# Kernel tuning notes

Hardware: AMD Instinct MI355X
Metric: run time of the kernel (lower is better)

## Reference

```python
import jax, jax.numpy as jnp
import numpy as np

B, N1, N2, D, H = 16, 1024, 1024, 1024, 16
DH = D // H  # head dim = 64
NEG = jnp.float32(-1e30)  # mask fill value (avoids -inf NaNs, bf16-safe)


def setup_inputs() -> dict:
    key = jax.random.key(0)
    ks = jax.random.split(key, 8)
    s = 0.02
    q = jax.random.normal(ks[0], (B, N1, D), dtype=jnp.float32)
    x = jax.random.normal(ks[1], (B, N2, D), dtype=jnp.float32)
    Wq = jax.random.normal(ks[2], (D, D), dtype=jnp.float32) * s
    Wk = jax.random.normal(ks[3], (D, D), dtype=jnp.float32) * s
    Wv = jax.random.normal(ks[4], (D, D), dtype=jnp.float32) * s
    Wo = jax.random.normal(ks[5], (D, D), dtype=jnp.float32) * s
    bq = jnp.zeros((D,), jnp.float32)
    bk = jnp.zeros((D,), jnp.float32)
    bv = jnp.zeros((D,), jnp.float32)
    bo = jnp.zeros((D,), jnp.float32)
    adj_mat = jax.random.randint(ks[6], (N1, N2), 0, 2).astype(jnp.bool_)
    return {"q": q, "x": x, "Wq": Wq, "bq": bq, "Wk": Wk, "bk": bk,
            "Wv": Wv, "bv": bv, "Wo": Wo, "bo": bo, "adj_mat": adj_mat}


def reference(q, x, Wq, bq, Wk, bk, Wv, bv, Wo, bo, adj_mat):
    b = q.shape[0]
    # QKV projections (torch Linear: y = x @ W.T + b), split into heads
    qh = (q @ Wq.T + bq).reshape(b, N1, H, DH).transpose(0, 2, 1, 3)  # [B,H,N1,DH]
    kh = (x @ Wk.T + bk).reshape(b, N2, H, DH).transpose(0, 2, 1, 3)  # [B,H,N2,DH]
    vh = (x @ Wv.T + bv).reshape(b, N2, H, DH).transpose(0, 2, 1, 3)  # [B,H,N2,DH]
    # masked SDPA with fixed adjacency mask (broadcast over batch & heads)
    scale = jnp.asarray(DH, qh.dtype) ** -0.5
    scores = jnp.einsum("bhqd,bhkd->bhqk", qh, kh) * scale           # [B,H,N1,N2]
    scores = jnp.where(adj_mat, scores, NEG)
    attn = jax.nn.softmax(scores, axis=-1)
    o = jnp.einsum("bhqk,bhkd->bhqd", attn, vh)                      # [B,H,N1,DH]
    o = o.transpose(0, 2, 1, 3).reshape(b, N1, D)
    return o @ Wo.T + bo
```

## Files before the change

### kernel.cpp

```cpp
#include <hip/hip_runtime.h>


typedef float f32x4 __attribute__((ext_vector_type(4)));
typedef float f32x16 __attribute__((ext_vector_type(16)));
typedef __bf16 bf16x8 __attribute__((ext_vector_type(8)));

#define QSCALE 0.18033688f

__device__ __forceinline__ unsigned short f2bf(float f) {
    unsigned u = __builtin_bit_cast(unsigned, f);
    unsigned r = u + 0x7fffu + ((u >> 16) & 1u);
    return (unsigned short)(r >> 16);
}
__device__ __forceinline__ unsigned pk2(float a, float b) {
    return (unsigned)f2bf(a) | ((unsigned)f2bf(b) << 16);
}

__global__ __launch_bounds__(256) void cvt_bf16(const float* __restrict__ s0,
                                                unsigned short* __restrict__ d0,
                                                const float* __restrict__ s1,
                                                unsigned short* __restrict__ d1) {
    const float* src = blockIdx.y ? s1 : s0;
    unsigned short* dst = blockIdx.y ? d1 : d0;
    const int idx = blockIdx.x * 256 + threadIdx.x;
    float4 a = ((const float4*)src)[idx * 2];
    float4 b = ((const float4*)src)[idx * 2 + 1];
    uint4 u;
    u.x = pk2(a.x, a.y); u.y = pk2(a.z, a.w);
    u.z = pk2(b.x, b.y); u.w = pk2(b.z, b.w);
    ((uint4*)dst)[idx] = u;
}

__global__ __launch_bounds__(256) void cvt_w4(const float* __restrict__ W0,
                                              const float* __restrict__ W1,
                                              const float* __restrict__ W2,
                                              const float* __restrict__ W3,
                                              unsigned short* __restrict__ o0,
                                              unsigned short* __restrict__ o1,
                                              unsigned short* __restrict__ o2,
                                              unsigned short* __restrict__ o3) {
    const float* s = (blockIdx.y == 0) ? W0 : (blockIdx.y == 1) ? W1
                   : (blockIdx.y == 2) ? W2 : W3;
    unsigned short* d = (blockIdx.y == 0) ? o0 : (blockIdx.y == 1) ? o1
                      : (blockIdx.y == 2) ? o2 : o3;
    const int idx = blockIdx.x * 256 + threadIdx.x;
    float4 a = ((const float4*)s)[idx * 2];
    float4 b = ((const float4*)s)[idx * 2 + 1];
    uint4 u;
    u.x = pk2(a.x, a.y); u.y = pk2(a.z, a.w);
    u.z = pk2(b.x, b.y); u.w = pk2(b.z, b.w);
    ((uint4*)d)[idx] = u;
}

template <int OUTM_CONST>
__device__ __forceinline__ void gemm_body(const unsigned short* __restrict__ A,
                                          const unsigned short* __restrict__ W,
                                          const float* __restrict__ bias,
                                          void* __restrict__ Cp,
                                          float scale, int b2, int outm_rt) {
    constexpr int N = 1024, K = 1024;
    __shared__ unsigned short As[2][128 * 64];
    __shared__ unsigned short Bs[2][128 * 64];

    const int t    = threadIdx.x;
    const int wave = t >> 6;
    const int lane = t & 63;
    const int xcd  = b2 & 7;
    const int jj   = b2 >> 3;
    const int n0   = (jj & 7) * 128;
    const int m0   = (xcd * 16 + (jj >> 3)) * 128;
    const int wr   = (wave >> 1) * 64;
    const int wc   = (wave & 1) * 64;
    const int lm   = lane & 15;
    const int quad = lane >> 4;

    int aoff[4], boff[4];
#pragma unroll
    for (int i = 0; i < 4; i++) {
        const int slot = wave * 256 + i * 64 + lane;
        const int r = slot >> 3;
        const int csrc = (slot & 7) ^ (r & 7);
        aoff[i] = (m0 + r) * K + csrc * 8;
        boff[i] = (n0 + r) * K + csrc * 8;
    }

    auto STAGE = [&](int cb, int k0) {
#pragma unroll
        for (int i = 0; i < 4; i++) {
            __builtin_amdgcn_global_load_lds(
                (const __attribute__((address_space(1))) unsigned int*)(A + aoff[i] + k0),
                (__attribute__((address_space(3))) unsigned int*)((char*)&As[cb][0] + wave * 4096 + i * 1024),
                16, 0, 0);
            __builtin_amdgcn_global_load_lds(
                (const __attribute__((address_space(1))) unsigned int*)(W + boff[i] + k0),
                (__attribute__((address_space(3))) unsigned int*)((char*)&Bs[cb][0] + wave * 4096 + i * 1024),
                16, 0, 0);
        }
    };

    f32x4 acc[4][4] = {};

    STAGE(0, 0);
    __syncthreads();

    int cur = 0;
    for (int k0 = 0; k0 < K; k0 += 64) {
        if (k0 + 64 < K) STAGE(cur ^ 1, k0 + 64);

        bf16x8 af[2][4], bfr[2][4];
#pragma unroll
        for (int ks = 0; ks < 2; ks++)
#pragma unroll
            for (int i = 0; i < 4; i++) {
                const int pos = ((ks * 4 + quad) ^ (lm & 7)) * 16;
                af[ks][i]  = *(const bf16x8*)((const char*)&As[cur][0] + (wr + i * 16 + lm) * 128 + pos);
                bfr[ks][i] = *(const bf16x8*)((const char*)&Bs[cur][0] + (wc + i * 16 + lm) * 128 + pos);
            }
        __builtin_amdgcn_s_setprio(1);
#pragma unroll
        for (int ks = 0; ks < 2; ks++)
#pragma unroll
            for (int i = 0; i < 4; i++)
#pragma unroll
                for (int j = 0; j < 4; j++)
                    acc[i][j] = __builtin_amdgcn_mfma_f32_16x16x32_bf16(af[ks][i], bfr[ks][j],
                                                                        acc[i][j], 0, 0, 0);
        __builtin_amdgcn_s_setprio(0);
        __syncthreads();
        cur ^= 1;
    }

    const int outm = (OUTM_CONST >= 0) ? OUTM_CONST : outm_rt;

#pragma unroll
    for (int i = 0; i < 4; i++) {
        const int row = m0 + wr + i * 16 + quad * 4;
#pragma unroll
        for (int j = 0; j < 4; j++) {
            const int col = n0 + wc + j * 16 + lm;
            const float bb = bias[col];
            if (outm == 2) {
                const int bi = row >> 10, n2 = row & 1023;
                const int hh = col >> 6, dh = col & 63;
                uint2 pkd;
                pkd.x = pk2((acc[i][j][0] + bb) * scale, (acc[i][j][1] + bb) * scale);
                pkd.y = pk2((acc[i][j][2] + bb) * scale, (acc[i][j][3] + bb) * scale);
                *(uint2*)&((unsigned short*)Cp)[((size_t)((bi * 16 + hh) * 64 + dh) << 10) + n2] = pkd;
            } else if (outm == 0) {
#pragma unroll
                for (int rr = 0; rr < 4; rr++)
                    ((unsigned short*)Cp)[(size_t)(row + rr) * N + col] =
                        f2bf((acc[i][j][rr] + bb) * scale);
            } else {
#pragma unroll
                for (int rr = 0; rr < 4; rr++)
                    ((float*)Cp)[(size_t)(row + rr) * N + col] = (acc[i][j][rr] + bb) * scale;
            }
        }
    }
}

__global__ __launch_bounds__(256, 2) void gemm_qkv(const unsigned short* __restrict__ qb,
                                                   const unsigned short* __restrict__ xb,
                                                   const unsigned short* __restrict__ Wqb,
                                                   const unsigned short* __restrict__ Wkb,
                                                   const unsigned short* __restrict__ Wvb,
                                                   const float* __restrict__ bq,
                                                   const float* __restrict__ bk,
                                                   const float* __restrict__ bv,
                                                   unsigned short* __restrict__ Qo,
                                                   unsigned short* __restrict__ Ko,
                                                   unsigned short* __restrict__ Vo) {
    const int bid = blockIdx.x;
    const int z   = bid >> 10;
    const int b2  = bid & 1023;
    const unsigned short* A = (z == 0) ? qb : xb;
    const unsigned short* W = (z == 0) ? Wqb : (z == 1) ? Wkb : Wvb;
    const float* bias       = (z == 0) ? bq : (z == 1) ? bk : bv;
    void* Cp                = (z == 0) ? (void*)Qo : (z == 1) ? (void*)Ko : (void*)Vo;
    const float scale       = (z == 0) ? QSCALE : 1.0f;
    gemm_body<-1>(A, W, bias, Cp, scale, b2, (z == 2) ? 2 : 0);
}

template <int OUTM>
__global__ __launch_bounds__(256, 2) void gemm2(const unsigned short* __restrict__ A,
                                                const unsigned short* __restrict__ W,
                                                const float* __restrict__ bias,
                                                void* __restrict__ Cp,
                                                float scale) {
    gemm_body<OUTM>(A, W, bias, Cp, scale, blockIdx.x, OUTM);
}

template <bool A_BF16, int OUTM>
__global__ __launch_bounds__(256) void gemm_bt(const void* __restrict__ Ap,
                                               const float* __restrict__ Wp,
                                               const float* __restrict__ bias,
                                               void* __restrict__ Cp,
                                               float scale) {
    constexpr int N = 1024, K = 1024;
    __shared__ unsigned short As[128 * 40];
    __shared__ unsigned short Bs[128 * 40];

    const int t    = threadIdx.x;
    const int n0   = blockIdx.x * 128;
    const int m0   = blockIdx.y * 128;
    const int wave = t >> 6;
    const int lane = t & 63;
    const int wr   = (wave >> 1) * 64;
    const int wc   = (wave & 1) * 64;
    const int lm   = lane & 15;
    const int quad = lane >> 4;
    const int kfr  = quad * 8;
    const int srow  = t >> 1;
    const int shalf = (t & 1) * 16;

    f32x4 acc[4][4] = {};

    for (int k0 = 0; k0 < K; k0 += 32) {
        {
            unsigned short* dst = &As[srow * 40 + shalf];
            if constexpr (A_BF16) {
                const unsigned short* pa =
                    (const unsigned short*)Ap + (size_t)(m0 + srow) * K + k0 + shalf;
                *(uint4*)dst       = *(const uint4*)pa;
                *(uint4*)(dst + 8) = *(const uint4*)(pa + 8);
            } else {
                const float* pa = (const float*)Ap + (size_t)(m0 + srow) * K + k0 + shalf;
                float4 f0 = *(const float4*)(pa + 0);
                float4 f1 = *(const float4*)(pa + 4);
                float4 f2 = *(const float4*)(pa + 8);
                float4 f3 = *(const float4*)(pa + 12);
                uint4 u0, u1;
                u0.x = pk2(f0.x, f0.y); u0.y = pk2(f0.z, f0.w);
                u0.z = pk2(f1.x, f1.y); u0.w = pk2(f1.z, f1.w);
                u1.x = pk2(f2.x, f2.y); u1.y = pk2(f2.z, f2.w);
                u1.z = pk2(f3.x, f3.y); u1.w = pk2(f3.z, f3.w);
                *(uint4*)dst       = u0;
                *(uint4*)(dst + 8) = u1;
            }
        }
        {
            const float* pb = Wp + (size_t)(n0 + srow) * K + k0 + shalf;
            float4 f0 = *(const float4*)(pb + 0);
            float4 f1 = *(const float4*)(pb + 4);
            float4 f2 = *(const float4*)(pb + 8);
            float4 f3 = *(const float4*)(pb + 12);
            uint4 u0, u1;
            u0.x = pk2(f0.x, f0.y); u0.y = pk2(f0.z, f0.w);
            u0.z = pk2(f1.x, f1.y); u0.w = pk2(f1.z, f1.w);
            u1.x = pk2(f2.x, f2.y); u1.y = pk2(f2.z, f2.w);
            u1.z = pk2(f3.x, f3.y); u1.w = pk2(f3.z, f3.w);
            unsigned short* dst = &Bs[srow * 40 + shalf];
            *(uint4*)dst       = u0;
            *(uint4*)(dst + 8) = u1;
        }
        __syncthreads();

        bf16x8 af[4], bfr[4];
#pragma unroll
        for (int i = 0; i < 4; i++)
            af[i] = *reinterpret_cast<const bf16x8*>(&As[(wr + i * 16 + lm) * 40 + kfr]);
#pragma unroll
        for (int j = 0; j < 4; j++)
            bfr[j] = *reinterpret_cast<const bf16x8*>(&Bs[(wc + j * 16 + lm) * 40 + kfr]);
#pragma unroll
        for (int i = 0; i < 4; i++)
#pragma unroll
            for (int j = 0; j < 4; j++)
                acc[i][j] = __builtin_amdgcn_mfma_f32_16x16x32_bf16(af[i], bfr[j],
                                                                    acc[i][j], 0, 0, 0);
        __syncthreads();
    }

#pragma unroll
    for (int i = 0; i < 4; i++) {
        const int row = m0 + wr + i * 16 + quad * 4;
#pragma unroll
        for (int j = 0; j < 4; j++) {
            const int col = n0 + wc + j * 16 + lm;
            const float bb = bias[col];
#pragma unroll
            for (int rr = 0; rr < 4; rr++) {
                const float v = (acc[i][j][rr] + bb) * scale;
                const int m = row + rr;
                if constexpr (OUTM == 0) {
                    ((unsigned short*)Cp)[(size_t)m * N + col] = f2bf(v);
                } else if constexpr (OUTM == 1) {
                    ((float*)Cp)[(size_t)m * N + col] = v;
                } else {
                    const int bi = m >> 10, n2 = m & 1023;
                    const int hh = col >> 6, dh = col & 63;
                    ((unsigned short*)Cp)[((size_t)((bi * 16 + hh) * 64 + dh) << 10) + n2] =
                        f2bf(v);
                }
            }
        }
    }
}

__global__ __launch_bounds__(256) void pack_adj(const int* __restrict__ adj,
                                                unsigned* __restrict__ adjm) {
    const int idx = blockIdx.x * 256 + threadIdx.x;
    const int* src = adj + (size_t)idx * 32;
    unsigned w = 0;
#pragma unroll
    for (int i = 0; i < 32; i++) w |= (src[i] != 0 ? 1u : 0u) << i;
    adjm[idx] = w;
}

__global__ __launch_bounds__(256, 3) void attn_kernel(const unsigned short* __restrict__ Q,
                                                      const unsigned short* __restrict__ K,
                                                      const unsigned short* __restrict__ Vt,
                                                      const unsigned* __restrict__ adjm,
                                                      unsigned short* __restrict__ O) {
    __shared__ unsigned short Kbuf[2][4096];
    __shared__ unsigned short Vbuf[2][4096];

    const int t    = threadIdx.x;
    const int wave = t >> 6;
    const int lane = t & 63;
    const int l32  = lane & 31;
    const int hi   = lane >> 5;

    const int bid   = blockIdx.x;
    const int xcd   = bid & 7;
    const int jj    = bid >> 3;
    const int group = xcd * 32 + (jj >> 3);
    const int q0    = (jj & 7) * 128;
    const int h     = group & 15;
    const int b     = group >> 4;

    const int qrow = q0 + wave * 32 + l32;

    int    ldofs[2];
    size_t kofs[2], vofs[2];
#pragma unroll
    for (int i = 0; i < 2; i++) {
        const int slot = i * 256 + t;
        const int r    = slot >> 3;
        const int cs   = (slot & 7) ^ (r & 7);
        ldofs[i] = slot * 16;
        kofs[i]  = (size_t)(b * 1024 + r) * 1024 + h * 64 + cs * 8;
        vofs[i]  = ((size_t)((b * 16 + h) * 64 + r) << 10) + cs * 8;
    }

    bf16x8 aq[4];
    {
        const unsigned short* qp =
            Q + ((size_t)(b * 1024 + qrow) * 1024 + h * 64 + hi * 8);
#pragma unroll
        for (int s = 0; s < 4; s++)
            aq[s] = __builtin_bit_cast(bf16x8, *(const uint4*)(qp + s * 16));
    }

    bf16x8 bones;
    {
        uint4 u; u.x = 0x3F803F80u; u.y = u.x; u.z = u.x; u.w = u.x;
        bones = __builtin_bit_cast(bf16x8, u);
    }

    f32x16 of0 = {}, of1 = {}, ol = {};

    auto STAGE = [&](int bi, int c) {
        const size_t j0 = (size_t)c * 64;
#pragma unroll
        for (int i = 0; i < 2; i++) {
            __builtin_amdgcn_global_load_lds(
                (const __attribute__((address_space(1))) unsigned int*)(K + kofs[i] + j0 * 1024),
                (__attribute__((address_space(3))) unsigned int*)((char*)&Kbuf[bi][0] + ldofs[i]),
                16, 0, 0);
            __builtin_amdgcn_global_load_lds(
                (const __attribute__((address_space(1))) unsigned int*)(Vt + vofs[i] + j0),
                (__attribute__((address_space(3))) unsigned int*)((char*)&Vbuf[bi][0] + ldofs[i]),
                16, 0, 0);
        }
    };

    STAGE(0, 0);
    __syncthreads();

    int bi = 0;
    for (int c = 0; c < 16; ++c) {
        const uint2 mw = *(const uint2*)&adjm[(size_t)qrow * 32 + c * 2];

        if (c < 15) STAGE(bi ^ 1, c + 1);

        f32x16 sf[2] = {{}, {}};
        __builtin_amdgcn_s_setprio(1);
#pragma unroll
        for (int f = 0; f < 2; f++)
#pragma unroll
            for (int s = 0; s < 4; s++) {
                const int pos = ((2 * s + hi) ^ (l32 & 7)) * 16;
                const bf16x8 kf =
                    *(const bf16x8*)((const char*)&Kbuf[bi][0] + (f * 32 + l32) * 128 + pos);
                sf[f] = __builtin_amdgcn_mfma_f32_32x32x16_bf16(kf, aq[s], sf[f], 0, 0, 0);
            }
        __builtin_amdgcn_s_setprio(0);

        unsigned d[2][4][2];
#pragma unroll
        for (int f = 0; f < 2; f++) {
            const unsigned wh = ((f == 0) ? mw.x : mw.y) >> (hi * 4);
            float p[16];
#pragma unroll
            for (int r = 0; r < 16; r++) {
                const unsigned bit = (wh >> ((r & 3) + 8 * (r >> 2))) & 1u;
                p[r] = __builtin_amdgcn_exp2f(bit ? sf[f][r] : -1e30f);
            }
#pragma unroll
            for (int a = 0; a < 4; a++)
#pragma unroll
                for (int bb = 0; bb < 2; bb++) {
                    unsigned dd;
                    asm("v_cvt_pk_bf16_f32 %0, %1, %2"
                        : "=v"(dd) : "v"(p[4 * a + 2 * bb]), "v"(p[4 * a + 2 * bb + 1]));
                    d[f][a][bb] = dd;
                }
        }

        bf16x8 tA[4];
#pragma unroll
        for (int s = 0; s < 4; s++) {
            const int f = s >> 1, sg = s & 1;
            unsigned A0 = d[f][2 * sg][0], B0 = d[f][2 * sg + 1][0];
            unsigned A1 = d[f][2 * sg][1], B1 = d[f][2 * sg + 1][1];
            asm("v_permlane32_swap_b32 %0, %1" : "+v"(A0), "+v"(B0));
            asm("v_permlane32_swap_b32 %0, %1" : "+v"(A1), "+v"(B1));
            uint4 td; td.x = A0; td.y = A1; td.z = B0; td.w = B1;
            tA[s] = __builtin_bit_cast(bf16x8, td);
        }

        __builtin_amdgcn_s_setprio(1);
#pragma unroll
        for (int s = 0; s < 4; s++) {
            const int pos = ((2 * s + hi) ^ (l32 & 7)) * 16;
            const bf16x8 v0 = *(const bf16x8*)((const char*)&Vbuf[bi][0] + l32 * 128 + pos);
            const bf16x8 v1 = *(const bf16x8*)((const char*)&Vbuf[bi][0] + (32 + l32) * 128 + pos);
            of0 = __builtin_amdgcn_mfma_f32_32x32x16_bf16(tA[s], v0, of0, 0, 0, 0);
            of1 = __builtin_amdgcn_mfma_f32_32x32x16_bf16(tA[s], v1, of1, 0, 0, 0);
            ol  = __builtin_amdgcn_mfma_f32_32x32x16_bf16(tA[s], bones, ol, 0, 0, 0);
        }
        __builtin_amdgcn_s_setprio(0);

        __syncthreads();
        bi ^= 1;
    }

#pragma unroll
    for (int r = 0; r < 16; r++) {
        const float iv = 1.0f / ol[r];
        const size_t row = (size_t)(b * 1024 + q0 + wave * 32 +
                                    (r & 3) + 8 * (r >> 2) + 4 * hi);
        unsigned short* op = O + row * 1024 + h * 64 + l32;
        op[0]  = f2bf(of0[r] * iv);
        op[32] = f2bf(of1[r] * iv);
    }
}

extern "C" void kernel_launch(void* const* d_in, const int* in_sizes, int n_in,
                              void* d_out, int out_size, void* d_ws, size_t ws_size,
                              hipStream_t stream) {
    const float* q  = (const float*)d_in[0];
    const float* x  = (const float*)d_in[1];
    const float* Wq = (const float*)d_in[2];
    const float* bq = (const float*)d_in[3];
    const float* Wk = (const float*)d_in[4];
    const float* bk = (const float*)d_in[5];
    const float* Wv = (const float*)d_in[6];
    const float* bv = (const float*)d_in[7];
    const float* Wo = (const float*)d_in[8];
    const float* bo = (const float*)d_in[9];
    const int* adj  = (const int*)d_in[10];
    float* out = (float*)d_out;

    const size_t MB = 1024 * 1024;
    char* w = (char*)d_ws;

    dim3 tb(256);
    const size_t FULL_WS = 168 * MB + 128 * 1024;

    if (ws_size >= FULL_WS) {
        unsigned short* qb  = (unsigned short*)(w);
        unsigned short* xb  = (unsigned short*)(w + 32 * MB);
        unsigned short* Wqb = (unsigned short*)(w + 64 * MB);
        unsigned short* Wkb = (unsigned short*)(w + 66 * MB);
        unsigned short* Wvb = (unsigned short*)(w + 68 * MB);
        unsigned short* Wob = (unsigned short*)(w + 70 * MB);
        unsigned short* Qb  = (unsigned short*)(w + 72 * MB);
        unsigned short* Kb  = (unsigned short*)(w + 104 * MB);
        unsigned short* Vtb = (unsigned short*)(w + 136 * MB);
        unsigned* adjm      = (unsigned*)(w + 168 * MB);
        unsigned short* Ob  = qb;

        hipLaunchKernelGGL(cvt_bf16, dim3(8192, 2), tb, 0, stream, q, qb, x, xb);
        hipLaunchKernelGGL(cvt_w4, dim3(512, 4), tb, 0, stream, Wq, Wk, Wv, Wo,
                           Wqb, Wkb, Wvb, Wob);
        hipLaunchKernelGGL(pack_adj, dim3(128), tb, 0, stream, adj, adjm);

        hipLaunchKernelGGL(gemm_qkv, dim3(3072), tb, 0, stream,
                           qb, xb, Wqb, Wkb, Wvb, bq, bk, bv, Qb, Kb, Vtb);
        hipLaunchKernelGGL(attn_kernel, dim3(2048), tb, 0, stream, Qb, Kb, Vtb, adjm, Ob);
        hipLaunchKernelGGL((gemm2<1>), dim3(1024), tb, 0, stream, Ob, Wob, bo, (void*)out, 1.0f);
    } else {
        unsigned short* Qb  = (unsigned short*)(w);
        unsigned short* Kb  = (unsigned short*)(w + 32 * MB);
        unsigned short* Vtb = (unsigned short*)(w + 64 * MB);
        unsigned short* Ob  = (unsigned short*)(w + 96 * MB);
        unsigned* adjm      = (unsigned*)(w + 128 * MB);

        hipLaunchKernelGGL(pack_adj, dim3(128), tb, 0, stream, adj, adjm);
        hipLaunchKernelGGL((gemm_bt<false, 0>), dim3(8, 128), tb, 0, stream,
                           (const void*)q, Wq, bq, (void*)Qb, QSCALE);
        hipLaunchKernelGGL((gemm_bt<false, 0>), dim3(8, 128), tb, 0, stream,
                           (const void*)x, Wk, bk, (void*)Kb, 1.0f);
        hipLaunchKernelGGL((gemm_bt<false, 2>), dim3(8, 128), tb, 0, stream,
                           (const void*)x, Wv, bv, (void*)Vtb, 1.0f);
        hipLaunchKernelGGL(attn_kernel, dim3(2048), tb, 0, stream, Qb, Kb, Vtb, adjm, Ob);
        hipLaunchKernelGGL((gemm_bt<true, 1>), dim3(8, 128), tb, 0, stream,
                           (const void*)Ob, Wo, bo, (void*)out, 1.0f);
    }
}
```

Before: 449.7 us.

## Fuse fp32-to-bf16 activation conversion into QKV GEMM and merge prep kernels

The separate pass that converts q and x to bf16 is removed. The QKV GEMM now loads fp32 activation tiles into registers, converts them, and writes swizzled bf16 into LDS after the MFMA loop. The weight conversion and adjacency packing are merged into one prep kernel to cut launches. This drops a 64MB read plus 64MB write round trip, but the GEMM now reads fp32 A tiles twice over (once per N-tile column, so 8x) and relies on register staging instead of async LDS loads for A.

```diff
diff --git a/kernel.cpp b/kernel.cpp
--- a/kernel.cpp
+++ b/kernel.cpp
@@ -16,48 +16,43 @@
     return (unsigned)f2bf(a) | ((unsigned)f2bf(b) << 16);
 }
 
-__global__ __launch_bounds__(256) void cvt_bf16(const float* __restrict__ s0,
-                                                unsigned short* __restrict__ d0,
-                                                const float* __restrict__ s1,
-                                                unsigned short* __restrict__ d1) {
-    const float* src = blockIdx.y ? s1 : s0;
-    unsigned short* dst = blockIdx.y ? d1 : d0;
-    const int idx = blockIdx.x * 256 + threadIdx.x;
-    float4 a = ((const float4*)src)[idx * 2];
-    float4 b = ((const float4*)src)[idx * 2 + 1];
-    uint4 u;
-    u.x = pk2(a.x, a.y); u.y = pk2(a.z, a.w);
-    u.z = pk2(b.x, b.y); u.w = pk2(b.z, b.w);
-    ((uint4*)dst)[idx] = u;
-}
-
-__global__ __launch_bounds__(256) void cvt_w4(const float* __restrict__ W0,
-                                              const float* __restrict__ W1,
-                                              const float* __restrict__ W2,
-                                              const float* __restrict__ W3,
-                                              unsigned short* __restrict__ o0,
-                                              unsigned short* __restrict__ o1,
-                                              unsigned short* __restrict__ o2,
-                                              unsigned short* __restrict__ o3) {
-    const float* s = (blockIdx.y == 0) ? W0 : (blockIdx.y == 1) ? W1
-                   : (blockIdx.y == 2) ? W2 : W3;
-    unsigned short* d = (blockIdx.y == 0) ? o0 : (blockIdx.y == 1) ? o1
-                      : (blockIdx.y == 2) ? o2 : o3;
-    const int idx = blockIdx.x * 256 + threadIdx.x;
-    float4 a = ((const float4*)s)[idx * 2];
-    float4 b = ((const float4*)s)[idx * 2 + 1];
-    uint4 u;
-    u.x = pk2(a.x, a.y); u.y = pk2(a.z, a.w);
-    u.z = pk2(b.x, b.y); u.w = pk2(b.z, b.w);
-    ((uint4*)d)[idx] = u;
-}
-
-template <int OUTM_CONST>
-__device__ __forceinline__ void gemm_body(const unsigned short* __restrict__ A,
-                                          const unsigned short* __restrict__ W,
-                                          const float* __restrict__ bias,
-                                          void* __restrict__ Cp,
-                                          float scale, int b2, int outm_rt) {
+__global__ __launch_bounds__(256) void prep(const float* __restrict__ W0,
+                                            const float* __restrict__ W1,
+                                            const float* __restrict__ W2,
+                                            const float* __restrict__ W3,
+                                            unsigned short* __restrict__ o0,
+                                            unsigned short* __restrict__ o1,
+                                            unsigned short* __restrict__ o2,
+                                            unsigned short* __restrict__ o3,
+                                            const int* __restrict__ adj,
+                                            unsigned* __restrict__ adjm) {
+    const int bid = blockIdx.x;
+    if (bid < 2048) {
+        const int wsel = bid >> 9;
+        const float* s = (wsel == 0) ? W0 : (wsel == 1) ? W1 : (wsel == 2) ? W2 : W3;
+        unsigned short* d = (wsel == 0) ? o0 : (wsel == 1) ? o1 : (wsel == 2) ? o2 : o3;
+        const int idx = (bid & 511) * 256 + threadIdx.x;
+        float4 a = ((const float4*)s)[idx * 2];
+        float4 b = ((const float4*)s)[idx * 2 + 1];
+        uint4 u;
+        u.x = pk2(a.x, a.y); u.y = pk2(a.z, a.w);
+        u.z = pk2(b.x, b.y); u.w = pk2(b.z, b.w);
+        ((uint4*)d)[idx] = u;
+    } else {
+        const int idx = (bid - 2048) * 256 + threadIdx.x;
+        const int* src = adj + (size_t)idx * 32;
+        unsigned w = 0;
+#pragma unroll
+        for (int i = 0; i < 32; i++) w |= (src[i] != 0 ? 1u : 0u) << i;
+        adjm[idx] = w;
+    }
+}
+
+__device__ __forceinline__ void gemm_f32a_body(const float* __restrict__ A,
+                                               const unsigned short* __restrict__ W,
+                                               const float* __restrict__ bias,
+                                               void* __restrict__ Cp,
+                                               float scale, int b2, int outm) {
     constexpr int N = 1024, K = 1024;
     __shared__ unsigned short As[2][128 * 64];
     __shared__ unsigned short Bs[2][128 * 64];
@@ -74,38 +69,61 @@
     const int lm   = lane & 15;
     const int quad = lane >> 4;
 
-    int aoff[4], boff[4];
+    const int srow = t >> 1;
+    const int colh = (t & 1) * 32;
+    const float* abase = A + (size_t)(m0 + srow) * K + colh;
+
+    int boff[4];
 #pragma unroll
     for (int i = 0; i < 4; i++) {
         const int slot = wave * 256 + i * 64 + lane;
         const int r = slot >> 3;
         const int csrc = (slot & 7) ^ (r & 7);
-        aoff[i] = (m0 + r) * K + csrc * 8;
         boff[i] = (n0 + r) * K + csrc * 8;
     }
 
-    auto STAGE = [&](int cb, int k0) {
-#pragma unroll
-        for (int i = 0; i < 4; i++) {
-            __builtin_amdgcn_global_load_lds(
-                (const __attribute__((address_space(1))) unsigned int*)(A + aoff[i] + k0),
-                (__attribute__((address_space(3))) unsigned int*)((char*)&As[cb][0] + wave * 4096 + i * 1024),
-                16, 0, 0);
+    float4 fa[8];
+    auto LOADA = [&](int k0) {
+#pragma unroll
+        for (int i = 0; i < 8; i++)
+            fa[i] = *(const float4*)(abase + k0 + i * 4);
+    };
+    auto WRITEA = [&](int cb) {
+        unsigned short* dst = &As[cb][srow * 64];
+#pragma unroll
+        for (int cc = 0; cc < 4; cc++) {
+            uint4 u;
+            u.x = pk2(fa[cc * 2].x, fa[cc * 2].y);
+            u.y = pk2(fa[cc * 2].z, fa[cc * 2].w);
+            u.z = pk2(fa[cc * 2 + 1].x, fa[cc * 2 + 1].y);
+            u.w = pk2(fa[cc * 2 + 1].z, fa[cc * 2 + 1].w);
+            const int c = (colh >> 3) + cc;
+            *(uint4*)(dst + ((c ^ (srow & 7)) * 8)) = u;
+        }
+    };
+    auto STAGEW = [&](int cb, int k0) {
+#pragma unroll
+        for (int i = 0; i < 4; i++)
             __builtin_amdgcn_global_load_lds(
                 (const __attribute__((address_space(1))) unsigned int*)(W + boff[i] + k0),
                 (__attribute__((address_space(3))) unsigned int*)((char*)&Bs[cb][0] + wave * 4096 + i * 1024),
                 16, 0, 0);
-        }
     };
 
     f32x4 acc[4][4] = {};
 
-    STAGE(0, 0);
+    LOADA(0);
+    STAGEW(0, 0);
+    WRITEA(0);
     __syncthreads();
 
     int cur = 0;
     for (int k0 = 0; k0 < K; k0 += 64) {
-        if (k0 + 64 < K) STAGE(cur ^ 1, k0 + 64);
+        const bool more = (k0 + 64 < K);
+        if (more) {
+            LOADA(k0 + 64);
+            STAGEW(cur ^ 1, k0 + 64);
+        }
 
         bf16x8 af[2][4], bfr[2][4];
 #pragma unroll
@@ -126,11 +144,11 @@
                     acc[i][j] = __builtin_amdgcn_mfma_f32_16x16x32_bf16(af[ks][i], bfr[ks][j],
                                                                         acc[i][j], 0, 0, 0);
         __builtin_amdgcn_s_setprio(0);
+
+        if (more) WRITEA(cur ^ 1);
         __syncthreads();
         cur ^= 1;
     }
-
-    const int outm = (OUTM_CONST >= 0) ? OUTM_CONST : outm_rt;
 
 #pragma unroll
     for (int i = 0; i < 4; i++) {
@@ -146,22 +164,18 @@
                 pkd.x = pk2((acc[i][j][0] + bb) * scale, (acc[i][j][1] + bb) * scale);
                 pkd.y = pk2((acc[i][j][2] + bb) * scale, (acc[i][j][3] + bb) * scale);
                 *(uint2*)&((unsigned short*)Cp)[((size_t)((bi * 16 + hh) * 64 + dh) << 10) + n2] = pkd;
-            } else if (outm == 0) {
+            } else {
 #pragma unroll
                 for (int rr = 0; rr < 4; rr++)
                     ((unsigned short*)Cp)[(size_t)(row + rr) * N + col] =
                         f2bf((acc[i][j][rr] + bb) * scale);
-            } else {
-#pragma unroll
-                for (int rr = 0; rr < 4; rr++)
-                    ((float*)Cp)[(size_t)(row + rr) * N + col] = (acc[i][j][rr] + bb) * scale;
             }
         }
     }
 }
 
-__global__ __launch_bounds__(256, 2) void gemm_qkv(const unsigned short* __restrict__ qb,
-                                                   const unsigned short* __restrict__ xb,
+__global__ __launch_bounds__(256, 2) void gemm_qkv(const float* __restrict__ q,
+                                                   const float* __restrict__ x,
                                                    const unsigned short* __restrict__ Wqb,
                                                    const unsigned short* __restrict__ Wkb,
                                                    const unsigned short* __restrict__ Wvb,
@@ -174,21 +188,104 @@
     const int bid = blockIdx.x;
     const int z   = bid >> 10;
     const int b2  = bid & 1023;
-    const unsigned short* A = (z == 0) ? qb : xb;
+    const float* A          = (z == 0) ? q : x;
     const unsigned short* W = (z == 0) ? Wqb : (z == 1) ? Wkb : Wvb;
     const float* bias       = (z == 0) ? bq : (z == 1) ? bk : bv;
     void* Cp                = (z == 0) ? (void*)Qo : (z == 1) ? (void*)Ko : (void*)Vo;
     const float scale       = (z == 0) ? QSCALE : 1.0f;
-    gemm_body<-1>(A, W, bias, Cp, scale, b2, (z == 2) ? 2 : 0);
-}
-
-template <int OUTM>
-__global__ __launch_bounds__(256, 2) void gemm2(const unsigned short* __restrict__ A,
-                                                const unsigned short* __restrict__ W,
-                                                const float* __restrict__ bias,
-                                                void* __restrict__ Cp,
-                                                float scale) {
-    gemm_body<OUTM>(A, W, bias, Cp, scale, blockIdx.x, OUTM);
+    gemm_f32a_body(A, W, bias, Cp, scale, b2, (z == 2) ? 2 : 0);
+}
+
+__global__ __launch_bounds__(256, 2) void gemm_o(const unsigned short* __restrict__ A,
+                                                 const unsigned short* __restrict__ W,
+                                                 const float* __restrict__ bias,
+                                                 float* __restrict__ Cp,
+                                                 float scale) {
+    constexpr int N = 1024, K = 1024;
+    __shared__ unsigned short As[2][128 * 64];
+    __shared__ unsigned short Bs[2][128 * 64];
+
+    const int t    = threadIdx.x;
+    const int wave = t >> 6;
+    const int lane = t & 63;
+    const int b2   = blockIdx.x;
+    const int xcd  = b2 & 7;
+    const int jj   = b2 >> 3;
+    const int n0   = (jj & 7) * 128;
+    const int m0   = (xcd * 16 + (jj >> 3)) * 128;
+    const int wr   = (wave >> 1) * 64;
+    const int wc   = (wave & 1) * 64;
+    const int lm   = lane & 15;
+    const int quad = lane >> 4;
+
+    int aoff[4], boff[4];
+#pragma unroll
+    for (int i = 0; i < 4; i++) {
+        const int slot = wave * 256 + i * 64 + lane;
+        const int r = slot >> 3;
+        const int csrc = (slot & 7) ^ (r & 7);
+        aoff[i] = (m0 + r) * K + csrc * 8;
+        boff[i] = (n0 + r) * K + csrc * 8;
+    }
+
+    auto STAGE = [&](int cb, int k0) {
+#pragma unroll
+        for (int i = 0; i < 4; i++) {
+            __builtin_amdgcn_global_load_lds(
+                (const __attribute__((address_space(1))) unsigned int*)(A + aoff[i] + k0),
+                (__attribute__((address_space(3))) unsigned int*)((char*)&As[cb][0] + wave * 4096 + i * 1024),
+                16, 0, 0);
+            __builtin_amdgcn_global_load_lds(
+                (const __attribute__((address_space(1))) unsigned int*)(W + boff[i] + k0),
+                (__attribute__((address_space(3))) unsigned int*)((char*)&Bs[cb][0] + wave * 4096 + i * 1024),
+                16, 0, 0);
+        }
+    };
+
+    f32x4 acc[4][4] = {};
+
+    STAGE(0, 0);
+    __syncthreads();
+
+    int cur = 0;
+    for (int k0 = 0; k0 < K; k0 += 64) {
+        if (k0 + 64 < K) STAGE(cur ^ 1, k0 + 64);
+
+        bf16x8 af[2][4], bfr[2][4];
+#pragma unroll
+        for (int ks = 0; ks < 2; ks++)
+#pragma unroll
+            for (int i = 0; i < 4; i++) {
+                const int pos = ((ks * 4 + quad) ^ (lm & 7)) * 16;
+                af[ks][i]  = *(const bf16x8*)((const char*)&As[cur][0] + (wr + i * 16 + lm) * 128 + pos);
+                bfr[ks][i] = *(const bf16x8*)((const char*)&Bs[cur][0] + (wc + i * 16 + lm) * 128 + pos);
+            }
+        __builtin_amdgcn_s_setprio(1);
+#pragma unroll
+        for (int ks = 0; ks < 2; ks++)
+#pragma unroll
+            for (int i = 0; i < 4; i++)
+#pragma unroll
+                for (int j = 0; j < 4; j++)
+                    acc[i][j] = __builtin_amdgcn_mfma_f32_16x16x32_bf16(af[ks][i], bfr[ks][j],
+                                                                        acc[i][j], 0, 0, 0);
+        __builtin_amdgcn_s_setprio(0);
+        __syncthreads();
+        cur ^= 1;
+    }
+
+#pragma unroll
+    for (int i = 0; i < 4; i++) {
+        const int row = m0 + wr + i * 16 + quad * 4;
+#pragma unroll
+        for (int j = 0; j < 4; j++) {
+            const int col = n0 + wc + j * 16 + lm;
+            const float bb = bias[col];
+#pragma unroll
+            for (int rr = 0; rr < 4; rr++)
+                Cp[(size_t)(row + rr) * N + col] = (acc[i][j][rr] + bb) * scale;
+        }
+    }
 }
 
 template <bool A_BF16, int OUTM>
@@ -481,8 +578,7 @@
     const size_t FULL_WS = 168 * MB + 128 * 1024;
 
     if (ws_size >= FULL_WS) {
-        unsigned short* qb  = (unsigned short*)(w);
-        unsigned short* xb  = (unsigned short*)(w + 32 * MB);
+        unsigned short* Ob  = (unsigned short*)(w);
         unsigned short* Wqb = (unsigned short*)(w + 64 * MB);
         unsigned short* Wkb = (unsigned short*)(w + 66 * MB);
         unsigned short* Wvb = (unsigned short*)(w + 68 * MB);
@@ -491,17 +587,13 @@
         unsigned short* Kb  = (unsigned short*)(w + 104 * MB);
         unsigned short* Vtb = (unsigned short*)(w + 136 * MB);
         unsigned* adjm      = (unsigned*)(w + 168 * MB);
-        unsigned short* Ob  = qb;
-
-        hipLaunchKernelGGL(cvt_bf16, dim3(8192, 2), tb, 0, stream, q, qb, x, xb);
-        hipLaunchKernelGGL(cvt_w4, dim3(512, 4), tb, 0, stream, Wq, Wk, Wv, Wo,
-                           Wqb, Wkb, Wvb, Wob);
-        hipLaunchKernelGGL(pack_adj, dim3(128), tb, 0, stream, adj, adjm);
-
+
+        hipLaunchKernelGGL(prep, dim3(2176), tb, 0, stream,
+                           Wq, Wk, Wv, Wo, Wqb, Wkb, Wvb, Wob, adj, adjm);
         hipLaunchKernelGGL(gemm_qkv, dim3(3072), tb, 0, stream,
-                           qb, xb, Wqb, Wkb, Wvb, bq, bk, bv, Qb, Kb, Vtb);
+                           q, x, Wqb, Wkb, Wvb, bq, bk, bv, Qb, Kb, Vtb);
         hipLaunchKernelGGL(attn_kernel, dim3(2048), tb, 0, stream, Qb, Kb, Vtb, adjm, Ob);
-        hipLaunchKernelGGL((gemm2<1>), dim3(1024), tb, 0, stream, Ob, Wob, bo, (void*)out, 1.0f);
+        hipLaunchKernelGGL(gemm_o, dim3(1024), tb, 0, stream, Ob, Wob, bo, out, 1.0f);
     } else {
         unsigned short* Qb  = (unsigned short*)(w);
         unsigned short* Kb  = (unsigned short*)(w + 32 * MB);
```

Result: slower. 610.8 us (+35.8%).
